# Optimization experiments

Hardware: AMD Instinct MI355X
Metric: run time of the kernel (lower is better)

The kernel has to match this reference:

```python
import jax, jax.numpy as jnp
import numpy as np

NU = 1.0  # degrees of freedom of the Student-t / Tsallis softmax


def setup_inputs() -> dict:
    key = jax.random.key(0)
    k1, k2, k3, k4 = jax.random.split(key, 4)
    B, Nx, Nh, Ny = 8192, 2048, 512, 1024
    x = jax.random.normal(k1, (B, Nx), dtype=jnp.float32)
    W_fc = jax.random.normal(k2, (Nh, Nx), dtype=jnp.float32) * (1.0 / np.sqrt(Nx))
    b_fc = jax.random.normal(k3, (Nh,), dtype=jnp.float32) * 0.01
    W_q = jax.random.normal(k4, (Ny, Nh), dtype=jnp.float32) * (1.0 / np.sqrt(Nh))
    return {"x": x, "W_fc": W_fc, "b_fc": b_fc, "W_q": W_q}


def reference(x, W_fc, b_fc, W_q):
    # x: [B, Nx] -> relu -> Linear(Nx, Nh) -> relu
    h = jax.nn.relu(jax.nn.relu(x) @ W_fc.T + b_fc)  # [B, Nh]
    # Quadratic layer: squared Euclidean distance to each class prototype.
    # ||h - w_j||^2 = ||h||^2 - 2 h.w_j + ||w_j||^2  (avoids [B, Ny, Nh] tensor)
    d = (jnp.sum(h * h, axis=-1, keepdims=True)
         - 2.0 * (h @ W_q.T)
         + jnp.sum(W_q * W_q, axis=-1))  # [B, Ny]
    d = jnp.maximum(d, 0.0)  # guard tiny negatives from fp cancellation
    # LogTSoftmax: p_j \propto (1 + d_j/nu)^{-(nu+1)/2}
    t = (-(NU + 1.0) / 2.0) * jnp.log1p(d / NU)  # [B, Ny]
    return t - jax.scipy.special.logsumexp(t, axis=-1, keepdims=True)
```

## Files before the change

### kernel.cpp

```cpp
#include <hip/hip_runtime.h>
#include <stdint.h>
#include <stddef.h>

#define B_ROWS 8192
#define NX 2048
#define NH 512
#define NY 1024

#define X_ELEMS (B_ROWS * NX)
#define EW_ELEMS (X_ELEMS + NH * NX)
#define EW_BLOCKS (EW_ELEMS / (8 * 256))
#define WQ_BLOCKS (NY / 4)

typedef __attribute__((ext_vector_type(8))) short bf16x8;
typedef __attribute__((ext_vector_type(4))) float f32x4;

static __device__ __forceinline__ unsigned short f2bf(float f) {
    union { float f; unsigned int u; } c; c.f = f;
    unsigned int r = 0x7FFFu + ((c.u >> 16) & 1u);
    return (unsigned short)((c.u + r) >> 16);
}

static __device__ __forceinline__ void glld16(const void* g, void* l) {
    __builtin_amdgcn_global_load_lds(
        (const __attribute__((address_space(1))) unsigned int*)g,
        (__attribute__((address_space(3))) unsigned int*)l, 16, 0, 0);
}

__global__ __launch_bounds__(256) void prep_kernel(const float* __restrict__ x,
                                                   const float* __restrict__ wfc,
                                                   const float* __restrict__ wq,
                                                   unsigned short* __restrict__ xb,
                                                   unsigned short* __restrict__ wfcb,
                                                   unsigned short* __restrict__ wqb,
                                                   float* __restrict__ wqsq,
                                                   float* __restrict__ hsq) {
    const int bid = blockIdx.x;
    const int tid = threadIdx.x;
    if (bid < EW_BLOCKS) {
        size_t idx = ((size_t)bid * 256 + tid) * 8;
        if (idx < (size_t)X_ELEMS) {
            float4 a = *(const float4*)&x[idx];
            float4 b = *(const float4*)&x[idx + 4];
            bf16x8 o;
            o[0] = (short)f2bf(fmaxf(a.x, 0.f)); o[1] = (short)f2bf(fmaxf(a.y, 0.f));
            o[2] = (short)f2bf(fmaxf(a.z, 0.f)); o[3] = (short)f2bf(fmaxf(a.w, 0.f));
            o[4] = (short)f2bf(fmaxf(b.x, 0.f)); o[5] = (short)f2bf(fmaxf(b.y, 0.f));
            o[6] = (short)f2bf(fmaxf(b.z, 0.f)); o[7] = (short)f2bf(fmaxf(b.w, 0.f));
            *(bf16x8*)&xb[idx] = o;
        } else {
            size_t off = idx - X_ELEMS;
            float4 a = *(const float4*)&wfc[off];
            float4 b = *(const float4*)&wfc[off + 4];
            bf16x8 o;
            o[0] = (short)f2bf(a.x); o[1] = (short)f2bf(a.y);
            o[2] = (short)f2bf(a.z); o[3] = (short)f2bf(a.w);
            o[4] = (short)f2bf(b.x); o[5] = (short)f2bf(b.y);
            o[6] = (short)f2bf(b.z); o[7] = (short)f2bf(b.w);
            *(bf16x8*)&wfcb[off] = o;
        }
    } else {
        const int b2 = bid - EW_BLOCKS;
        const int lane = tid & 63;
        const int row = b2 * 4 + (tid >> 6);
        const float* p = wq + (size_t)row * NH + lane * 8;
        float4 a = *(const float4*)p;
        float4 b = *(const float4*)(p + 4);
        bf16x8 o;
        o[0] = (short)f2bf(a.x); o[1] = (short)f2bf(a.y);
        o[2] = (short)f2bf(a.z); o[3] = (short)f2bf(a.w);
        o[4] = (short)f2bf(b.x); o[5] = (short)f2bf(b.y);
        o[6] = (short)f2bf(b.z); o[7] = (short)f2bf(b.w);
        *(bf16x8*)&wqb[(size_t)row * NH + lane * 8] = o;
        float s = a.x*a.x + a.y*a.y + a.z*a.z + a.w*a.w
                + b.x*b.x + b.y*b.y + b.z*b.z + b.w*b.w;
        #pragma unroll
        for (int off = 32; off > 0; off >>= 1) s += __shfl_xor(s, off);
        if (lane == 0) wqsq[row] = s;
        if (tid < 32) hsq[b2 * 32 + tid] = 0.0f;
    }
}

__global__ __launch_bounds__(512, 2) void gemm1_kernel(const unsigned short* __restrict__ xb,
                                                       const unsigned short* __restrict__ wfcb,
                                                       const float* __restrict__ b_fc,
                                                       unsigned short* __restrict__ hb,
                                                       float* __restrict__ hsq) {
    __shared__ unsigned char smem[65536];
    unsigned char* AsB = smem;
    unsigned char* BsB = smem + 32768;

    const int tid = threadIdx.x;
    const int lane = tid & 63;
    const int grp = tid >> 8;
    const int wave = (tid >> 6) & 3;
    const int wm = wave >> 1, wn = wave & 1;
    const int quad = lane >> 4;
    const int r = lane & 15;

    const int bid = blockIdx.x;
    const int n0 = ((bid >> 3) & 3) * 128;
    const int m0 = (((bid & 7) << 3) | (bid >> 5)) * 128;
    const int kbase = grp * (NX / 2);

    f32x4 acc[4][4];
    #pragma unroll
    for (int i = 0; i < 4; ++i)
        #pragma unroll
        for (int j = 0; j < 4; ++j) acc[i][j] = (f32x4)(0.0f);

    const int lrow = lane >> 2;
    const int gch = (lane & 3) ^ ((lrow >> 1) & 3);
    const char* xbB = (const char*)xb;
    const char* wfB = (const char*)wfcb;
    const int fsw = (quad ^ ((r >> 1) & 3)) * 16;

    auto stage = [&](int buf, int k0) {
        const int sb = grp * 16384 + buf * 8192;
        #pragma unroll
        for (int c = 0; c < 2; ++c) {
            int R0 = wave * 32 + c * 16;
            glld16(xbB + (size_t)(m0 + R0 + lrow) * (NX * 2) + k0 * 2 + gch * 16,
                   AsB + sb + R0 * 64);
            glld16(wfB + (size_t)(n0 + R0 + lrow) * (NX * 2) + k0 * 2 + gch * 16,
                   BsB + sb + R0 * 64);
        }
    };

    stage(0, kbase);
    #pragma unroll 1
    for (int it = 0; it < 32; ++it) {
        __syncthreads();
        if (it + 1 < 32) stage((it + 1) & 1, kbase + it * 32 + 32);
        const unsigned char* ab = AsB + grp * 16384 + (it & 1) * 8192;
        const unsigned char* bb = BsB + grp * 16384 + (it & 1) * 8192;
        bf16x8 af[4], bfv[4];
        #pragma unroll
        for (int i = 0; i < 4; ++i)
            af[i] = *(const bf16x8*)(ab + (wm * 64 + i * 16 + r) * 64 + fsw);
        #pragma unroll
        for (int j = 0; j < 4; ++j)
            bfv[j] = *(const bf16x8*)(bb + (wn * 64 + j * 16 + r) * 64 + fsw);
        #pragma unroll
        for (int i = 0; i < 4; ++i)
            #pragma unroll
            for (int j = 0; j < 4; ++j)
                acc[i][j] = __builtin_amdgcn_mfma_f32_16x16x32_bf16(af[i], bfv[j], acc[i][j], 0, 0, 0);
    }

    float* smemF = (float*)smem;
    __syncthreads();
    if (grp == 1) {
        #pragma unroll
        for (int i = 0; i < 4; ++i) {
            #pragma unroll
            for (int j = 0; j < 4; ++j) {
                int cl = wn * 64 + j * 16 + r;
                int rowb = wm * 64 + i * 16 + quad * 4;
                *(f32x4*)(smemF + cl * 128 + (rowb ^ ((cl & 7) << 2))) = acc[i][j];
            }
        }
    }
    __syncthreads();
    if (grp == 0) {
        float p[4][4];
        #pragma unroll
        for (int i = 0; i < 4; ++i)
            #pragma unroll
            for (int rr = 0; rr < 4; ++rr) p[i][rr] = 0.0f;

        #pragma unroll
        for (int i = 0; i < 4; ++i) {
            #pragma unroll
            for (int j = 0; j < 4; ++j) {
                int cl = wn * 64 + j * 16 + r;
                int rowb = wm * 64 + i * 16 + quad * 4;
                f32x4 o = *(const f32x4*)(smemF + cl * 128 + (rowb ^ ((cl & 7) << 2)));
                int col = n0 + cl;
                float bias = b_fc[col];
                #pragma unroll
                for (int rr = 0; rr < 4; ++rr) {
                    float v = fmaxf(acc[i][j][rr] + o[rr] + bias, 0.0f);
                    hb[(size_t)(m0 + rowb + rr) * NH + col] = f2bf(v);
                    p[i][rr] += v * v;
                }
            }
        }
        #pragma unroll
        for (int mask = 1; mask < 16; mask <<= 1) {
            #pragma unroll
            for (int i = 0; i < 4; ++i)
                #pragma unroll
                for (int rr = 0; rr < 4; ++rr)
                    p[i][rr] += __shfl_xor(p[i][rr], mask);
        }
        if (r == 0) {
            #pragma unroll
            for (int i = 0; i < 4; ++i)
                #pragma unroll
                for (int rr = 0; rr < 4; ++rr)
                    atomicAdd(&hsq[m0 + wm * 64 + i * 16 + quad * 4 + rr], p[i][rr]);
        }
    }
}

__global__ __launch_bounds__(256, 2) void gemm2_kernel(const unsigned short* __restrict__ hb,
                                                       const unsigned short* __restrict__ wqb,
                                                       const float* __restrict__ hsq,
                                                       const float* __restrict__ wqsq,
                                                       float* __restrict__ out) {
    __shared__ unsigned short As[2 * 128 * 64];
    __shared__ unsigned short Bs[2 * 128 * 64];

    const int tid = threadIdx.x;
    const int lane = tid & 63;
    const int wave = tid >> 6;
    const int wm = wave >> 1, wn = wave & 1;
    const int quad = lane >> 4;
    const int r = lane & 15;

    const int bid = blockIdx.x;
    const int n0 = ((bid >> 3) & 7) * 128;
    const int m0 = (((bid & 7) << 3) | (bid >> 6)) * 128;

    f32x4 acc[4][4];
    #pragma unroll
    for (int i = 0; i < 4; ++i)
        #pragma unroll
        for (int j = 0; j < 4; ++j) acc[i][j] = (f32x4)(0.0f);

    const int lrow = lane >> 3;
    const int gch = (lane & 7) ^ lrow;
    const char* hbB = (const char*)hb;
    const char* wqB = (const char*)wqb;
    char* AsB = (char*)As;
    char* BsB = (char*)Bs;
    const int xk = r & 7;

    auto stage = [&](int buf, int k0) {
        #pragma unroll
        for (int c = 0; c < 4; ++c) {
            int R0 = wave * 32 + c * 8;
            glld16(hbB + (size_t)(m0 + R0 + lrow) * (NH * 2) + k0 * 2 + gch * 16,
                   AsB + buf * 16384 + R0 * 128);
            glld16(wqB + (size_t)(n0 + R0 + lrow) * (NH * 2) + k0 * 2 + gch * 16,
                   BsB + buf * 16384 + R0 * 128);
        }
    };

    stage(0, 0);
    #pragma unroll 1
    for (int it = 0; it < NH / 64; ++it) {
        const int k0 = it * 64;
        __syncthreads();
        if (it + 1 < NH / 64) stage((it + 1) & 1, k0 + 64);
        const char* ap = AsB + (it & 1) * 16384 + (wm * 64 + r) * 128;
        const char* bp = BsB + (it & 1) * 16384 + (wn * 64 + r) * 128;
        #pragma unroll
        for (int s = 0; s < 2; ++s) {
            const int ch = ((s * 4 + quad) ^ xk) * 16;
            bf16x8 af[4], bfv[4];
            #pragma unroll
            for (int i = 0; i < 4; ++i) af[i] = *(const bf16x8*)(ap + i * 16 * 128 + ch);
            #pragma unroll
            for (int j = 0; j < 4; ++j) bfv[j] = *(const bf16x8*)(bp + j * 16 * 128 + ch);
            #pragma unroll
            for (int i = 0; i < 4; ++i)
                #pragma unroll
                for (int j = 0; j < 4; ++j)
                    acc[i][j] = __builtin_amdgcn_mfma_f32_16x16x32_bf16(af[i], bfv[j], acc[i][j], 0, 0, 0);
        }
    }

    float hs[4][4];
    #pragma unroll
    for (int i = 0; i < 4; ++i)
        #pragma unroll
        for (int rr = 0; rr < 4; ++rr)
            hs[i][rr] = hsq[m0 + wm * 64 + i * 16 + quad * 4 + rr];

    #pragma unroll
    for (int i = 0; i < 4; ++i) {
        #pragma unroll
        for (int j = 0; j < 4; ++j) {
            int col = n0 + wn * 64 + j * 16 + r;
            float wq = wqsq[col];
            #pragma unroll
            for (int rr = 0; rr < 4; ++rr) {
                int row = m0 + wm * 64 + i * 16 + quad * 4 + rr;
                float d = hs[i][rr] - 2.0f * acc[i][j][rr] + wq;
                d = fmaxf(d, 0.0f);
                out[(size_t)row * NY + col] = -__logf(1.0f + d);
            }
        }
    }
}

__global__ __launch_bounds__(256) void lse_kernel(float* __restrict__ out) {
    __shared__ float reds[4];
    const int tid = threadIdx.x;
    const int lane = tid & 63;
    const int wave = tid >> 6;
    float* p = out + (size_t)blockIdx.x * NY;
    float4 v = ((const float4*)p)[tid];
    float s = __expf(v.x) + __expf(v.y) + __expf(v.z) + __expf(v.w);
    #pragma unroll
    for (int off = 32; off > 0; off >>= 1) s += __shfl_xor(s, off);
    if (lane == 0) reds[wave] = s;
    __syncthreads();
    float lse = __logf(reds[0] + reds[1] + reds[2] + reds[3]);
    v.x -= lse; v.y -= lse; v.z -= lse; v.w -= lse;
    ((float4*)p)[tid] = v;
}

extern "C" void kernel_launch(void* const* d_in, const int* in_sizes, int n_in,
                              void* d_out, int out_size, void* d_ws, size_t ws_size,
                              hipStream_t stream) {
    const float* x    = (const float*)d_in[0];
    const float* W_fc = (const float*)d_in[1];
    const float* b_fc = (const float*)d_in[2];
    const float* W_q  = (const float*)d_in[3];
    float* out = (float*)d_out;

    char* ws = (char*)d_ws;
    unsigned short* xb   = (unsigned short*)(ws);
    unsigned short* wfcb = (unsigned short*)(ws + 33554432);
    unsigned short* wqb  = (unsigned short*)(ws + 35651584);
    float*          wqsq = (float*)(ws + 36700160);
    unsigned short* hb   = (unsigned short*)(ws + 36704256);
    float*          hsq  = (float*)(ws + 45092864);

    prep_kernel<<<EW_BLOCKS + WQ_BLOCKS, 256, 0, stream>>>(x, W_fc, W_q, xb, wfcb, wqb, wqsq, hsq);
    gemm1_kernel<<<256, 512, 0, stream>>>(xb, wfcb, b_fc, hb, hsq);
    gemm2_kernel<<<512, 256, 0, stream>>>(hb, wqb, hsq, wqsq, out);
    lse_kernel<<<B_ROWS, 256, 0, stream>>>(out);
}
```

Baseline: 167.8 us.

## Fuse log-softmax into second GEMM with full-row tiles per block

Retiles gemm2 so each 512-thread block computes 32 complete output rows across all 1024 columns. That lets the row log-sum-exp be reduced in-kernel and the separate lse_kernel pass be dropped. Because NU=1, exp(t) equals 1/(1+d), so the sum is built with reciprocals instead of exp. This removes a full read and write of the output, but uses a large shared-memory buffer (about 132 KB per block) and a K step of 32, which limits occupancy and adds more barriers.

```diff
diff --git a/kernel.cpp b/kernel.cpp
--- a/kernel.cpp
+++ b/kernel.cpp
@@ -204,113 +204,129 @@
     }
 }
 
-__global__ __launch_bounds__(256, 2) void gemm2_kernel(const unsigned short* __restrict__ hb,
+__global__ __launch_bounds__(512, 2) void gemm2_kernel(const unsigned short* __restrict__ hb,
                                                        const unsigned short* __restrict__ wqb,
                                                        const float* __restrict__ hsq,
                                                        const float* __restrict__ wqsq,
                                                        float* __restrict__ out) {
-    __shared__ unsigned short As[2 * 128 * 64];
-    __shared__ unsigned short Bs[2 * 128 * 64];
+    __shared__ unsigned char smem[135168];
+    char* AsB = (char*)smem;
+    char* BsB = (char*)smem + 4096;
 
     const int tid = threadIdx.x;
     const int lane = tid & 63;
     const int wave = tid >> 6;
-    const int wm = wave >> 1, wn = wave & 1;
     const int quad = lane >> 4;
     const int r = lane & 15;
-
-    const int bid = blockIdx.x;
-    const int n0 = ((bid >> 3) & 7) * 128;
-    const int m0 = (((bid & 7) << 3) | (bid >> 6)) * 128;
-
-    f32x4 acc[4][4];
-    #pragma unroll
-    for (int i = 0; i < 4; ++i)
-        #pragma unroll
-        for (int j = 0; j < 4; ++j) acc[i][j] = (f32x4)(0.0f);
-
-    const int lrow = lane >> 3;
-    const int gch = (lane & 7) ^ lrow;
-    const char* hbB = (const char*)hb;
-    const char* wqB = (const char*)wqb;
-    char* AsB = (char*)As;
-    char* BsB = (char*)Bs;
-    const int xk = r & 7;
+    const int m0 = blockIdx.x * 32;
+
+    f32x4 acc[2][8];
+    #pragma unroll
+    for (int i = 0; i < 2; ++i)
+        #pragma unroll
+        for (int j = 0; j < 8; ++j) acc[i][j] = (f32x4)(0.0f);
+
+    const int lrow = lane >> 2;
+    const int gch = (lane & 3) ^ ((lrow >> 1) & 3);
+    const char* bsrc = (const char*)wqb + (size_t)(wave * 128 + lrow) * (NH * 2) + gch * 16;
+    const char* asrc = (const char*)hb + (size_t)(m0 + wave * 16 + lrow) * (NH * 2) + gch * 16;
+    const int fsw = (quad ^ ((r >> 1) & 3)) * 16;
 
     auto stage = [&](int buf, int k0) {
         #pragma unroll
-        for (int c = 0; c < 4; ++c) {
-            int R0 = wave * 32 + c * 8;
-            glld16(hbB + (size_t)(m0 + R0 + lrow) * (NH * 2) + k0 * 2 + gch * 16,
-                   AsB + buf * 16384 + R0 * 128);
-            glld16(wqB + (size_t)(n0 + R0 + lrow) * (NH * 2) + k0 * 2 + gch * 16,
-                   BsB + buf * 16384 + R0 * 128);
-        }
+        for (int c = 0; c < 8; ++c)
+            glld16(bsrc + (size_t)k0 * 2 + c * 16384,
+                   BsB + buf * 65536 + wave * 8192 + c * 1024);
+        if (wave < 2)
+            glld16(asrc + (size_t)k0 * 2, AsB + buf * 2048 + wave * 1024);
     };
 
     stage(0, 0);
     #pragma unroll 1
-    for (int it = 0; it < NH / 64; ++it) {
-        const int k0 = it * 64;
+    for (int it = 0; it < NH / 32; ++it) {
         __syncthreads();
-        if (it + 1 < NH / 64) stage((it + 1) & 1, k0 + 64);
-        const char* ap = AsB + (it & 1) * 16384 + (wm * 64 + r) * 128;
-        const char* bp = BsB + (it & 1) * 16384 + (wn * 64 + r) * 128;
-        #pragma unroll
-        for (int s = 0; s < 2; ++s) {
-            const int ch = ((s * 4 + quad) ^ xk) * 16;
-            bf16x8 af[4], bfv[4];
-            #pragma unroll
-            for (int i = 0; i < 4; ++i) af[i] = *(const bf16x8*)(ap + i * 16 * 128 + ch);
-            #pragma unroll
-            for (int j = 0; j < 4; ++j) bfv[j] = *(const bf16x8*)(bp + j * 16 * 128 + ch);
-            #pragma unroll
-            for (int i = 0; i < 4; ++i)
-                #pragma unroll
-                for (int j = 0; j < 4; ++j)
-                    acc[i][j] = __builtin_amdgcn_mfma_f32_16x16x32_bf16(af[i], bfv[j], acc[i][j], 0, 0, 0);
-        }
-    }
-
-    float hs[4][4];
-    #pragma unroll
-    for (int i = 0; i < 4; ++i)
+        if (it + 1 < NH / 32) stage((it + 1) & 1, it * 32 + 32);
+        const char* ab = AsB + (it & 1) * 2048;
+        const char* bb = BsB + (it & 1) * 65536 + wave * 8192;
+        bf16x8 af[2], bfv[8];
+        #pragma unroll
+        for (int i = 0; i < 2; ++i)
+            af[i] = *(const bf16x8*)(ab + (i * 16 + r) * 64 + fsw);
+        #pragma unroll
+        for (int j = 0; j < 8; ++j)
+            bfv[j] = *(const bf16x8*)(bb + (j * 16 + r) * 64 + fsw);
+        #pragma unroll
+        for (int i = 0; i < 2; ++i)
+            #pragma unroll
+            for (int j = 0; j < 8; ++j)
+                acc[i][j] = __builtin_amdgcn_mfma_f32_16x16x32_bf16(af[i], bfv[j], acc[i][j], 0, 0, 0);
+    }
+
+    float hs_[2][4];
+    #pragma unroll
+    for (int i = 0; i < 2; ++i)
         #pragma unroll
         for (int rr = 0; rr < 4; ++rr)
-            hs[i][rr] = hsq[m0 + wm * 64 + i * 16 + quad * 4 + rr];
-
-    #pragma unroll
-    for (int i = 0; i < 4; ++i) {
-        #pragma unroll
-        for (int j = 0; j < 4; ++j) {
-            int col = n0 + wn * 64 + j * 16 + r;
-            float wq = wqsq[col];
+            hs_[i][rr] = hsq[m0 + i * 16 + quad * 4 + rr];
+
+    float srow[2][4];
+    #pragma unroll
+    for (int i = 0; i < 2; ++i)
+        #pragma unroll
+        for (int rr = 0; rr < 4; ++rr) srow[i][rr] = 0.0f;
+
+    #pragma unroll
+    for (int j = 0; j < 8; ++j) {
+        float wqv = wqsq[wave * 128 + j * 16 + r];
+        #pragma unroll
+        for (int i = 0; i < 2; ++i) {
             #pragma unroll
             for (int rr = 0; rr < 4; ++rr) {
-                int row = m0 + wm * 64 + i * 16 + quad * 4 + rr;
-                float d = hs[i][rr] - 2.0f * acc[i][j][rr] + wq;
+                float d = hs_[i][rr] - 2.0f * acc[i][j][rr] + wqv;
                 d = fmaxf(d, 0.0f);
-                out[(size_t)row * NY + col] = -__logf(1.0f + d);
+                float onepd = 1.0f + d;
+                srow[i][rr] += __builtin_amdgcn_rcpf(onepd);
+                acc[i][j][rr] = -__logf(onepd);
             }
         }
     }
-}
-
-__global__ __launch_bounds__(256) void lse_kernel(float* __restrict__ out) {
-    __shared__ float reds[4];
-    const int tid = threadIdx.x;
-    const int lane = tid & 63;
-    const int wave = tid >> 6;
-    float* p = out + (size_t)blockIdx.x * NY;
-    float4 v = ((const float4*)p)[tid];
-    float s = __expf(v.x) + __expf(v.y) + __expf(v.z) + __expf(v.w);
-    #pragma unroll
-    for (int off = 32; off > 0; off >>= 1) s += __shfl_xor(s, off);
-    if (lane == 0) reds[wave] = s;
-    __syncthreads();
-    float lse = __logf(reds[0] + reds[1] + reds[2] + reds[3]);
-    v.x -= lse; v.y -= lse; v.z -= lse; v.w -= lse;
-    ((float4*)p)[tid] = v;
+    #pragma unroll
+    for (int mask = 1; mask < 16; mask <<= 1)
+        #pragma unroll
+        for (int i = 0; i < 2; ++i)
+            #pragma unroll
+            for (int rr = 0; rr < 4; ++rr)
+                srow[i][rr] += __shfl_xor(srow[i][rr], mask);
+
+    float* smemF = (float*)smem;
+    __syncthreads();
+    if (r == 0) {
+        #pragma unroll
+        for (int i = 0; i < 2; ++i)
+            #pragma unroll
+            for (int rr = 0; rr < 4; ++rr)
+                smemF[wave * 32 + i * 16 + quad * 4 + rr] = srow[i][rr];
+    }
+    __syncthreads();
+    if (tid < 32) {
+        float S = 0.0f;
+        #pragma unroll
+        for (int w = 0; w < 8; ++w) S += smemF[w * 32 + tid];
+        smemF[256 + tid] = __logf(S);
+    }
+    __syncthreads();
+
+    #pragma unroll
+    for (int i = 0; i < 2; ++i) {
+        #pragma unroll
+        for (int rr = 0; rr < 4; ++rr) {
+            float l = smemF[256 + i * 16 + quad * 4 + rr];
+            size_t rowoff = (size_t)(m0 + i * 16 + quad * 4 + rr) * NY + wave * 128 + r;
+            #pragma unroll
+            for (int j = 0; j < 8; ++j)
+                out[rowoff + j * 16] = acc[i][j][rr] - l;
+        }
+    }
 }
 
 extern "C" void kernel_launch(void* const* d_in, const int* in_sizes, int n_in,
@@ -332,6 +348,5 @@
 
     prep_kernel<<<EW_BLOCKS + WQ_BLOCKS, 256, 0, stream>>>(x, W_fc, W_q, xb, wfcb, wqb, wqsq, hsq);
     gemm1_kernel<<<256, 512, 0, stream>>>(xb, wfcb, b_fc, hb, hsq);
-    gemm2_kernel<<<512, 256, 0, stream>>>(hb, wqb, hsq, wqsq, out);
-    lse_kernel<<<B_ROWS, 256, 0, stream>>>(out);
-}
+    gemm2_kernel<<<B_ROWS / 32, 512, 0, stream>>>(hb, wqb, hsq, wqsq, out);
+}
```

Measured after the change: 173.2 us. 1.03x slower.
